# Performance work log

Measured on AMD Instinct MI355X. Metric: run time of the kernel, lower is better.

## Reference

```python
import jax, jax.numpy as jnp
import numpy as np

B, S, E, C = 128, 512, 768, 9


def setup_inputs() -> dict:
    key = jax.random.key(0)
    ks = jax.random.split(key, 7)
    return {
        "enc": jax.random.normal(ks[0], (B, S, E), dtype=jnp.float32),
        "W": jax.random.normal(ks[1], (C, E), dtype=jnp.float32) * 0.02,
        "b": jax.random.normal(ks[2], (C,), dtype=jnp.float32) * 0.02,
        "start_transitions": jax.random.normal(ks[3], (C,), dtype=jnp.float32) * 0.1,
        "end_transitions": jax.random.normal(ks[4], (C,), dtype=jnp.float32) * 0.1,
        "transitions": jax.random.normal(ks[5], (C, C), dtype=jnp.float32) * 0.1,
        "tags": jax.random.randint(ks[6], (B, S), 0, C, dtype=jnp.int64),
        "mask": jnp.ones((B, S), dtype=bool),
    }


def _crf_nll_mean(emissions, tags, mask, start_transitions, end_transitions, transitions):
    # emissions: [B,S,C], tags: [B,S] int, mask: [B,S] bool (mask[:,0] all True)
    maskf = mask.astype(emissions.dtype)
    b_idx = jnp.arange(emissions.shape[0])
    # ---- numerator: score of the gold tag path ----
    em_tag = jnp.take_along_axis(emissions, tags[..., None], axis=2)[..., 0]  # [B,S]
    trans_pair = transitions[tags[:, :-1], tags[:, 1:]]  # [B,S-1]
    num = start_transitions[tags[:, 0]] + em_tag[:, 0]
    num = num + jnp.sum((trans_pair + em_tag[:, 1:]) * maskf[:, 1:], axis=1)
    seq_len = mask.sum(axis=1).astype(jnp.int32)
    last_tags = tags[b_idx, seq_len - 1]
    num = num + end_transitions[last_tags]
    # ---- denominator: forward algorithm (log partition) via scan ----
    def step(alpha, xs):
        em_t, m_t = xs  # [B,C], [B]
        # broadcast: alpha[b,i] + transitions[i,j] + em_t[b,j]
        nxt = jax.nn.logsumexp(alpha[:, :, None] + transitions[None, :, :] + em_t[:, None, :], axis=1)
        alpha = jnp.where(m_t[:, None], nxt, alpha)
        return alpha, None

    alpha0 = start_transitions[None, :] + emissions[:, 0]  # [B,C]
    em_rest = jnp.swapaxes(emissions[:, 1:], 0, 1)  # [S-1,B,C]
    m_rest = jnp.swapaxes(mask[:, 1:], 0, 1)        # [S-1,B]
    alpha, _ = jax.lax.scan(step, alpha0, (em_rest, m_rest))
    den = jax.nn.logsumexp(alpha + end_transitions[None, :], axis=1)  # [B]
    # reduction='mean' over batch; module returns -llh
    return jnp.mean(den - num)


def reference(enc, W, b, start_transitions, end_transitions, transitions, tags, mask):
    # BERT output `enc` is frozen (torch.no_grad); dropout omitted (deterministic ref)
    emissions = jnp.einsum("bse,ce->bsc", enc, W) + b  # linear head [B,S,C]
    return _crf_nll_mean(emissions, tags, mask, start_transitions, end_transitions, transitions)
```

## Files before the change

kernel.cpp:

```cpp
#include <hip/hip_runtime.h>

static constexpr int kB = 128;
static constexpr int kS = 512;
static constexpr int kE = 768;
static constexpr int kC = 9;
static constexpr int kT = 16;
static constexpr int kChunks = 32;
static constexpr int kWpad = kE + 8;

using bf16x8 = __attribute__((ext_vector_type(8))) short;
using f32x4  = __attribute__((ext_vector_type(4))) float;

__device__ __forceinline__ unsigned short f2bf(float f) {
  union { float f; unsigned u; } cv; cv.f = f;
  return (unsigned short)((cv.u + 0x7FFFu + ((cv.u >> 16) & 1u)) >> 16);
}

__global__ __launch_bounds__(128) void fused_chunk(
    const float* __restrict__ enc, const float* __restrict__ W,
    const float* __restrict__ bias, const float* __restrict__ trans,
    const float* __restrict__ start_t, const float* __restrict__ end_t,
    const int* __restrict__ tags, float* __restrict__ Pout,
    float* __restrict__ numP) {
  __shared__ unsigned short Wl[16 * kWpad];
  __shared__ float emt[kT * 12];
  __shared__ float P[81];
  __shared__ float atmp[16];
  __shared__ float nred[kT];

  const int blk = blockIdx.x;
  const int b = blk >> 5;
  const int k = blk & 31;
  const int tid = threadIdx.x;

  for (int idx = tid; idx < kC * kE; idx += 128) {
    const int c = idx / kE, e = idx - c * kE;
    Wl[c * kWpad + e] = f2bf(W[idx]);
  }
  __syncthreads();

  if (tid < 64) {
    const int mn = tid & 15;
    const int quad = tid >> 4;
    const float* rp = enc + ((size_t)(b * kS + k * kT + mn)) * kE + quad * 8;
    const unsigned short* wp = Wl + mn * kWpad + quad * 8;
    f32x4 acc = {0.f, 0.f, 0.f, 0.f};
#pragma unroll
    for (int s = 0; s < kE / 32; ++s) {
      const float4 x0 = *reinterpret_cast<const float4*>(rp + s * 32);
      const float4 x1 = *reinterpret_cast<const float4*>(rp + s * 32 + 4);
      bf16x8 a;
      a[0] = (short)f2bf(x0.x); a[1] = (short)f2bf(x0.y);
      a[2] = (short)f2bf(x0.z); a[3] = (short)f2bf(x0.w);
      a[4] = (short)f2bf(x1.x); a[5] = (short)f2bf(x1.y);
      a[6] = (short)f2bf(x1.z); a[7] = (short)f2bf(x1.w);
      const bf16x8 bf = *reinterpret_cast<const bf16x8*>(wp + s * 32);
      acc = __builtin_amdgcn_mfma_f32_16x16x32_bf16(a, bf, acc, 0, 0, 0);
    }
    if (mn < kC) {
      const float bc = bias[mn];
#pragma unroll
      for (int r = 0; r < 4; ++r) emt[(quad * 4 + r) * 12 + mn] = acc[r] + bc;
    }
  }
  __syncthreads();

  if (tid < kT) {
    const int t = k * kT + tid;
    const int ct = tags[b * kS + t];
    float v = emt[tid * 12 + ct];
    if (t == 0) v += start_t[ct];
    else        v += trans[tags[b * kS + t - 1] * kC + ct];
    if (t == kS - 1) v += end_t[ct];
    nred[tid] = v;
  }
  __syncthreads();
  if (tid == 0) {
    float s = 0.f;
#pragma unroll
    for (int i = 0; i < kT; ++i) s += nred[i];
    numP[blk] = s;
  }

  const bool act = tid < 81;
  const int ci = act ? (tid / 9) : 0;
  const int cj = act ? (tid - ci * 9) : 0;
  float tr[kC];
  if (act) {
#pragma unroll
    for (int kk = 0; kk < kC; ++kk) tr[kk] = trans[kk * kC + cj];
  }

  if (k == 0) {
    if (tid < kC) atmp[tid] = start_t[tid] + emt[tid];
    __syncthreads();
    for (int t = 1; t < kT; ++t) {
      float nv = 0.f;
      if (tid < kC) {
        float m = -3.0e38f, v[kC];
#pragma unroll
        for (int i = 0; i < kC; ++i) { v[i] = atmp[i] + tr[i]; m = fmaxf(m, v[i]); }
        float s = 0.f;
#pragma unroll
        for (int i = 0; i < kC; ++i) s += __expf(v[i] - m);
        nv = m + __logf(s) + emt[t * 12 + tid];
      }
      __syncthreads();
      if (tid < kC) atmp[tid] = nv;
      __syncthreads();
    }
    if (tid < kC) Pout[(size_t)blk * 81 + tid] = atmp[tid];
  } else {
    if (act) P[tid] = trans[ci * kC + cj] + emt[cj];
    __syncthreads();
    for (int t = 1; t < kT; ++t) {
      float nv = 0.f;
      if (act) {
        float m = -3.0e38f, v[kC];
#pragma unroll
        for (int kk = 0; kk < kC; ++kk) { v[kk] = P[ci * 9 + kk] + tr[kk]; m = fmaxf(m, v[kk]); }
        float s = 0.f;
#pragma unroll
        for (int kk = 0; kk < kC; ++kk) s += __expf(v[kk] - m);
        nv = m + __logf(s) + emt[t * 12 + cj];
      }
      __syncthreads();
      if (act) P[tid] = nv;
      __syncthreads();
    }
    if (act) Pout[(size_t)blk * 81 + cj * kC + ci] = P[tid];
  }
}

__global__ __launch_bounds__(64) void combine_kernel(const float* __restrict__ Pmat,
                                                     const float* __restrict__ end_t,
                                                     float* __restrict__ den_out) {
  const int b = blockIdx.x;
  const int lane = threadIdx.x;
  if (lane >= kC) return;

  const float* Pb = Pmat + (size_t)b * kChunks * 81;
  float alpha = Pb[lane];

  for (int k = 1; k < kChunks; ++k) {
    const float* Pk = Pb + k * 81 + lane * kC;
    float p[kC];
#pragma unroll
    for (int i = 0; i < kC; ++i) p[i] = Pk[i];
    float tv[kC];
    float m = -3.0e38f;
#pragma unroll
    for (int i = 0; i < kC; ++i) {
      const float ai = __shfl(alpha, i, 64);
      tv[i] = ai + p[i];
      m = fmaxf(m, tv[i]);
    }
    float s = 0.f;
#pragma unroll
    for (int i = 0; i < kC; ++i) s += __expf(tv[i] - m);
    alpha = m + __logf(s);
  }

  const float v = alpha + end_t[lane];
  float vv[kC];
  float m = -3.0e38f;
#pragma unroll
  for (int i = 0; i < kC; ++i) {
    vv[i] = __shfl(v, i, 64);
    m = fmaxf(m, vv[i]);
  }
  float s = 0.f;
#pragma unroll
  for (int i = 0; i < kC; ++i) s += __expf(vv[i] - m);
  if (lane == 0) den_out[b] = m + __logf(s);
}

__global__ __launch_bounds__(128) void final_kernel(const float* __restrict__ den,
                                                    const float* __restrict__ numP,
                                                    float* __restrict__ out) {
  const int tid = threadIdx.x;
  float s = 0.f;
#pragma unroll
  for (int k = 0; k < kChunks; ++k) s += numP[tid * kChunks + k];
  float v = den[tid] - s;
#pragma unroll
  for (int m = 32; m >= 1; m >>= 1) v += __shfl_down(v, m, 64);
  __shared__ float sm[2];
  if ((tid & 63) == 0) sm[tid >> 6] = v;
  __syncthreads();
  if (tid == 0) out[0] = (sm[0] + sm[1]) * (1.0f / (float)kB);
}

extern "C" void kernel_launch(void* const* d_in, const int* in_sizes, int n_in,
                              void* d_out, int out_size, void* d_ws, size_t ws_size,
                              hipStream_t stream) {
  const float* enc   = (const float*)d_in[0];
  const float* W     = (const float*)d_in[1];
  const float* bias  = (const float*)d_in[2];
  const float* start = (const float*)d_in[3];
  const float* end_t = (const float*)d_in[4];
  const float* trans = (const float*)d_in[5];
  const int*   tags  = (const int*)d_in[6];

  float* Pmat = (float*)d_ws;
  float* numP = Pmat + (size_t)kB * kChunks * 81;
  float* den  = numP + kB * kChunks;
  float* out  = (float*)d_out;

  hipLaunchKernelGGL(fused_chunk, dim3(kB * kChunks), dim3(128), 0, stream,
                     enc, W, bias, trans, start, end_t, tags, Pmat, numP);
  hipLaunchKernelGGL(combine_kernel, dim3(kB), dim3(64), 0, stream, Pmat, end_t, den);
  hipLaunchKernelGGL(final_kernel, dim3(1), dim3(128), 0, stream, den, numP, out);
}
```

Before: 327.7 us.

## Precompute bf16 weights once and split the K-reduction across two waves

Adds a small kernel that converts W to bf16, padded to 16 rows, in workspace. This removes the per-block reconversion of W into LDS, which was redundant across 4096 blocks and wasted LDS. The emission GEMM now uses both waves, each reducing half of E, and the partials are summed when read. The combine kernel also prefetches the next chunk's matrix row. The cost is an extra launch, plus global or L2 reads of the bf16 W rows in place of LDS.

```diff
diff --git a/kernel.cpp b/kernel.cpp
--- a/kernel.cpp
+++ b/kernel.cpp
@@ -6,7 +6,6 @@
 static constexpr int kC = 9;
 static constexpr int kT = 16;
 static constexpr int kChunks = 32;
-static constexpr int kWpad = kE + 8;
 
 using bf16x8 = __attribute__((ext_vector_type(8))) short;
 using f32x4  = __attribute__((ext_vector_type(4))) float;
@@ -16,14 +15,19 @@
   return (unsigned short)((cv.u + 0x7FFFu + ((cv.u >> 16) & 1u)) >> 16);
 }
 
+__global__ __launch_bounds__(256) void wconv_kernel(const float* __restrict__ W,
+                                                    unsigned short* __restrict__ Wbf) {
+  const int idx = blockIdx.x * 256 + threadIdx.x;
+  if (idx < 16 * kE) Wbf[idx] = (idx < kC * kE) ? f2bf(W[idx]) : (unsigned short)0;
+}
+
 __global__ __launch_bounds__(128) void fused_chunk(
-    const float* __restrict__ enc, const float* __restrict__ W,
+    const float* __restrict__ enc, const unsigned short* __restrict__ Wbf,
     const float* __restrict__ bias, const float* __restrict__ trans,
     const float* __restrict__ start_t, const float* __restrict__ end_t,
     const int* __restrict__ tags, float* __restrict__ Pout,
     float* __restrict__ numP) {
-  __shared__ unsigned short Wl[16 * kWpad];
-  __shared__ float emt[kT * 12];
+  __shared__ float emt[2 * kT * 12];
   __shared__ float P[81];
   __shared__ float atmp[16];
   __shared__ float nred[kT];
@@ -32,21 +36,17 @@
   const int b = blk >> 5;
   const int k = blk & 31;
   const int tid = threadIdx.x;
-
-  for (int idx = tid; idx < kC * kE; idx += 128) {
-    const int c = idx / kE, e = idx - c * kE;
-    Wl[c * kWpad + e] = f2bf(W[idx]);
-  }
-  __syncthreads();
-
-  if (tid < 64) {
-    const int mn = tid & 15;
-    const int quad = tid >> 4;
-    const float* rp = enc + ((size_t)(b * kS + k * kT + mn)) * kE + quad * 8;
-    const unsigned short* wp = Wl + mn * kWpad + quad * 8;
+  const int wv = tid >> 6;
+  const int lane = tid & 63;
+  const int mn = lane & 15;
+  const int quad = lane >> 4;
+
+  {
+    const float* rp = enc + ((size_t)(b * kS + k * kT + mn)) * kE + wv * (kE / 2) + quad * 8;
+    const unsigned short* wp = Wbf + mn * kE + wv * (kE / 2) + quad * 8;
     f32x4 acc = {0.f, 0.f, 0.f, 0.f};
-#pragma unroll
-    for (int s = 0; s < kE / 32; ++s) {
+#pragma unroll 4
+    for (int s = 0; s < (kE / 2) / 32; ++s) {
       const float4 x0 = *reinterpret_cast<const float4*>(rp + s * 32);
       const float4 x1 = *reinterpret_cast<const float4*>(rp + s * 32 + 4);
       bf16x8 a;
@@ -58,17 +58,20 @@
       acc = __builtin_amdgcn_mfma_f32_16x16x32_bf16(a, bf, acc, 0, 0, 0);
     }
     if (mn < kC) {
-      const float bc = bias[mn];
-#pragma unroll
-      for (int r = 0; r < 4; ++r) emt[(quad * 4 + r) * 12 + mn] = acc[r] + bc;
+      const float bc = (wv == 0) ? bias[mn] : 0.f;
+#pragma unroll
+      for (int r = 0; r < 4; ++r)
+        emt[wv * (kT * 12) + (quad * 4 + r) * 12 + mn] = acc[r] + bc;
     }
   }
   __syncthreads();
+
+#define EM(t, c) (emt[(t) * 12 + (c)] + emt[kT * 12 + (t) * 12 + (c)])
 
   if (tid < kT) {
     const int t = k * kT + tid;
     const int ct = tags[b * kS + t];
-    float v = emt[tid * 12 + ct];
+    float v = EM(tid, ct);
     if (t == 0) v += start_t[ct];
     else        v += trans[tags[b * kS + t - 1] * kC + ct];
     if (t == kS - 1) v += end_t[ct];
@@ -92,7 +95,7 @@
   }
 
   if (k == 0) {
-    if (tid < kC) atmp[tid] = start_t[tid] + emt[tid];
+    if (tid < kC) atmp[tid] = start_t[tid] + EM(0, tid);
     __syncthreads();
     for (int t = 1; t < kT; ++t) {
       float nv = 0.f;
@@ -103,7 +106,7 @@
         float s = 0.f;
 #pragma unroll
         for (int i = 0; i < kC; ++i) s += __expf(v[i] - m);
-        nv = m + __logf(s) + emt[t * 12 + tid];
+        nv = m + __logf(s) + EM(t, tid);
       }
       __syncthreads();
       if (tid < kC) atmp[tid] = nv;
@@ -111,7 +114,7 @@
     }
     if (tid < kC) Pout[(size_t)blk * 81 + tid] = atmp[tid];
   } else {
-    if (act) P[tid] = trans[ci * kC + cj] + emt[cj];
+    if (act) P[tid] = trans[ci * kC + cj] + EM(0, cj);
     __syncthreads();
     for (int t = 1; t < kT; ++t) {
       float nv = 0.f;
@@ -122,7 +125,7 @@
         float s = 0.f;
 #pragma unroll
         for (int kk = 0; kk < kC; ++kk) s += __expf(v[kk] - m);
-        nv = m + __logf(s) + emt[t * 12 + cj];
+        nv = m + __logf(s) + EM(t, cj);
       }
       __syncthreads();
       if (act) P[tid] = nv;
@@ -130,6 +133,7 @@
     }
     if (act) Pout[(size_t)blk * 81 + cj * kC + ci] = P[tid];
   }
+#undef EM
 }
 
 __global__ __launch_bounds__(64) void combine_kernel(const float* __restrict__ Pmat,
@@ -142,11 +146,17 @@
   const float* Pb = Pmat + (size_t)b * kChunks * 81;
   float alpha = Pb[lane];
 
+  float p[kC];
+#pragma unroll
+  for (int i = 0; i < kC; ++i) p[i] = Pb[81 + lane * kC + i];
+
   for (int k = 1; k < kChunks; ++k) {
-    const float* Pk = Pb + k * 81 + lane * kC;
-    float p[kC];
-#pragma unroll
-    for (int i = 0; i < kC; ++i) p[i] = Pk[i];
+    float pn[kC];
+    if (k + 1 < kChunks) {
+      const float* Pn = Pb + (k + 1) * 81 + lane * kC;
+#pragma unroll
+      for (int i = 0; i < kC; ++i) pn[i] = Pn[i];
+    }
     float tv[kC];
     float m = -3.0e38f;
 #pragma unroll
@@ -159,6 +169,8 @@
 #pragma unroll
     for (int i = 0; i < kC; ++i) s += __expf(tv[i] - m);
     alpha = m + __logf(s);
+#pragma unroll
+    for (int i = 0; i < kC; ++i) p[i] = pn[i];
   }
 
   const float v = alpha + end_t[lane];
@@ -202,13 +214,15 @@
   const float* trans = (const float*)d_in[5];
   const int*   tags  = (const int*)d_in[6];
 
-  float* Pmat = (float*)d_ws;
+  unsigned short* Wbf = (unsigned short*)d_ws;
+  float* Pmat = (float*)((char*)d_ws + 16 * kE * sizeof(unsigned short));
   float* numP = Pmat + (size_t)kB * kChunks * 81;
   float* den  = numP + kB * kChunks;
   float* out  = (float*)d_out;
 
+  hipLaunchKernelGGL(wconv_kernel, dim3((16 * kE + 255) / 256), dim3(256), 0, stream, W, Wbf);
   hipLaunchKernelGGL(fused_chunk, dim3(kB * kChunks), dim3(128), 0, stream,
-                     enc, W, bias, trans, start, end_t, tags, Pmat, numP);
+                     enc, Wbf, bias, trans, start, end_t, tags, Pmat, numP);
   hipLaunchKernelGGL(combine_kernel, dim3(kB), dim3(64), 0, stream, Pmat, end_t, den);
   hipLaunchKernelGGL(final_kernel, dim3(1), dim3(128), 0, stream, den, numP, out);
 }
```

Result: faster. 308.2 us (-6.0%).
